# Kernel tuning notes

Hardware: AMD Instinct MI355X
Metric: run time of the kernel (lower is better)

## Reference

```python
import jax, jax.numpy as jnp
import numpy as np

N_EDGES, ADJ_K, EPROP_DIM = 50000, 9, 8
B, L = 512, 128
Z_DIM, T_DIM, TE_DIM, XE_DIM, H_DIM, O_DIM = 16, 48, 32, 128, 128, 32


def setup_inputs() -> dict:
    ks = jax.random.split(jax.random.key(0), 28)
    f = lambda k, s: jax.random.normal(k, s, jnp.float32) * 0.05
    in0 = Z_DIM + TE_DIM + XE_DIM + EPROP_DIM  # LSTM layer-0 input dim = 184
    mk_dim = XE_DIM + TE_DIM + EPROP_DIM       # 168
    return {
        "x": jax.random.randint(ks[0], (B, L), 0, N_EDGES),
        "dpt": jax.random.randint(ks[1], (B, L), 0, T_DIM),
        "z": jax.random.normal(ks[2], (L, B, Z_DIM), jnp.float32),
        "adj": jax.random.randint(ks[3], (N_EDGES, ADJ_K), 0, N_EDGES),
        "eprop": f(ks[4], (N_EDGES, EPROP_DIM)),
        "x_emb": f(ks[5], (N_EDGES, XE_DIM)),
        "t_emb": f(ks[6], (T_DIM, TE_DIM)),
        "tcost_emb": f(ks[7], (N_EDGES, TE_DIM)),
        "w_ih0": f(ks[8], (4 * H_DIM, in0)),
        "w_hh0": f(ks[9], (4 * H_DIM, H_DIM)),
        "b_ih0": f(ks[10], (4 * H_DIM,)),
        "b_hh0": f(ks[11], (4 * H_DIM,)),
        "w_ih1": f(ks[12], (4 * H_DIM, H_DIM)),
        "w_hh1": f(ks[13], (4 * H_DIM, H_DIM)),
        "b_ih1": f(ks[14], (4 * H_DIM,)),
        "b_hh1": f(ks[15], (4 * H_DIM,)),
        "w_ih2": f(ks[16], (4 * H_DIM, H_DIM)),
        "w_hh2": f(ks[17], (4 * H_DIM, H_DIM)),
        "b_ih2": f(ks[18], (4 * H_DIM,)),
        "b_hh2": f(ks[19], (4 * H_DIM,)),
        "wax": f(ks[20], (O_DIM, H_DIM)),
        "bax": f(ks[21], (O_DIM,)),
        "wat": f(ks[22], (O_DIM, 2 * TE_DIM)),
        "bat": f(ks[23], (O_DIM,)),
        "wmx": f(ks[24], (O_DIM, mk_dim)),
        "bmx": f(ks[25], (O_DIM,)),
        "wmt": f(ks[26], (O_DIM, mk_dim)),
        "bmt": f(ks[27], (O_DIM,)),
    }


def _lstm_cell(x, h, c, w_ih, w_hh, b_ih, b_hh):
    # PyTorch LSTMCell: gates ordered (i, f, g, o)
    g = x @ w_ih.T + b_ih + h @ w_hh.T + b_hh
    i, f, gg, o = jnp.split(g, 4, axis=-1)
    c = jax.nn.sigmoid(f) * c + jax.nn.sigmoid(i) * jnp.tanh(gg)
    h = jax.nn.sigmoid(o) * jnp.tanh(c)
    return h, c


def _forward(x, dpt, z, adj, eprop, x_emb, t_emb, tcost_emb,
             w_ih0, w_hh0, b_ih0, b_hh0, w_ih1, w_hh1, b_ih1, b_hh1,
             w_ih2, w_hh2, b_ih2, b_hh2, wax, bax, wat, bat, wmx, bmx, wmt, bmt):
    Bb = x.shape[0]
    N, K = adj.shape
    mask_id = N  # adj.size(0) + config.ADJ_MASK with ADJ_MASK=0 (pad id; never a valid node)
    H = w_hh0.shape[1]
    zro = lambda: jnp.zeros((Bb, H), x_emb.dtype)
    init = (zro(), zro(), zro(), zro(), zro(), zro())

    def step(carry, inp):
        h0, c0, h1, c1, h2, c2 = carry
        xt, dt, zt = inp                                   # [B], [B], [B,z]
        tt = t_emb[dt]                                     # [B,te]
        hid = jnp.concatenate([zt, x_emb[xt], tt, eprop[xt]], -1)
        h0, c0 = _lstm_cell(hid, h0, c0, w_ih0, w_hh0, b_ih0, b_hh0)
        h1, c1 = _lstm_cell(h0, h1, c1, w_ih1, w_hh1, b_ih1, b_hh1)
        h2, c2 = _lstm_cell(h1, h2, c2, w_ih2, w_hh2, b_ih2, b_hh2)
        afterx = jax.nn.relu(h2 @ wax.T + bax)             # [B,o]
        adjs = adj[xt]                                     # [B,K]
        ttb = jnp.broadcast_to(tt[:, None, :], (Bb, K, tt.shape[-1]))
        aftert = jax.nn.relu(jnp.concatenate([tcost_emb[adjs], ttb], -1) @ wat.T + bat)  # [B,K,o]
        mk = jnp.concatenate([x_emb[adjs], ttb, eprop[adjs]], -1)  # [B,K,xe+te+P]
        px = jnp.einsum('bo,bko->bk', afterx, mk @ wmx.T + bmx)    # [B,K]
        px = jnp.where(adjs == mask_id, -jnp.inf, px)
        pt = jnp.sum(aftert * (mk @ wmt.T + bmt), -1)              # [B,K]
        out = (jax.nn.log_softmax(px, -1), jax.nn.sigmoid(pt))
        return (h0, c0, h1, c1, h2, c2), out

    _, (pred_x, pred_t) = jax.lax.scan(step, init, (x.T, dpt.T, z))
    # torch stacks along dim 1 -> [B,L,K] then .view(-1,K)
    pred_x = jnp.transpose(pred_x, (1, 0, 2)).reshape(-1, K)
    pred_t = jnp.transpose(pred_t, (1, 0, 2)).reshape(-1, K)
    return pred_x, pred_t


def reference(x, dpt, z, adj, eprop, x_emb, t_emb, tcost_emb,
              w_ih0, w_hh0, b_ih0, b_hh0, w_ih1, w_hh1, b_ih1, b_hh1,
              w_ih2, w_hh2, b_ih2, b_hh2, wax, bax, wat, bat, wmx, bmx, wmt, bmt):
    return _forward(x, dpt, z, adj, eprop, x_emb, t_emb, tcost_emb,
                    w_ih0, w_hh0, b_ih0, b_hh0, w_ih1, w_hh1, b_ih1, b_hh1,
                    w_ih2, w_hh2, b_ih2, b_hh2, wax, bax, wat, bat, wmx, bmx, wmt, bmt)
```

## Files before the change

### kernel.cpp

```cpp
#include <hip/hip_runtime.h>
#include <hip/hip_fp16.h>
#include <math.h>
#include <stdint.h>

#define B_   512
#define L_   128
#define K_   9
#define NE   50000
#define ZD   16
#define TE   32
#define XE   128
#define EP   8
#define H_   128
#define G4   512
#define OD   32
#define IN0  184
#define MKD  168

typedef uint32_t u32;
typedef _Float16 half2v __attribute__((ext_vector_type(2)));
typedef _Float16 half8  __attribute__((ext_vector_type(8)));
typedef float    f32x4  __attribute__((ext_vector_type(4)));

__device__ __forceinline__ float sigm(float x) {
    x = fminf(fmaxf(x, -30.f), 30.f);
    return 1.f / (1.f + expf(-x));
}
__device__ __forceinline__ float tanh_f(float x) {
    x = fminf(fmaxf(x, -15.f), 15.f);
    float e = expf(2.f * x);
    return (e - 1.f) / (e + 1.f);
}
__device__ __forceinline__ float dot2f(u32 w, u32 h, float acc) {
#if __has_builtin(__builtin_amdgcn_fdot2)
    union { u32 u; half2v v; } a, b;
    a.u = w; b.u = h;
    return __builtin_amdgcn_fdot2(a.v, b.v, acc, false);
#else
    union { u32 u; __half2 h2; } a, b;
    a.u = w; b.u = h;
    float2 fa = __half22float2(a.h2), fb = __half22float2(b.h2);
    return fmaf(fa.x, fb.x, fmaf(fa.y, fb.y, acc));
#endif
}
__device__ __forceinline__ float dot4(uint4 w, uint4 h, float acc) {
    acc = dot2f(w.x, h.x, acc); acc = dot2f(w.y, h.y, acc);
    acc = dot2f(w.z, h.z, acc); acc = dot2f(w.w, h.w, acc);
    return acc;
}
__device__ __forceinline__ u32 packh(float lo, float hi) {
    union { __half2 h; u32 u; } p;
    p.h = __halves2half2(__float2half(lo), __float2half(hi));
    return p.u;
}
__device__ __forceinline__ f32x4 cvt4h(u32 a_, u32 b_) {
    union { u32 u; half2v v; } a, b;
    a.u = a_; b.u = b_;
    f32x4 r;
    r[0] = (float)a.v[0]; r[1] = (float)a.v[1];
    r[2] = (float)b.v[0]; r[3] = (float)b.v[1];
    return r;
}

__global__ void __launch_bounds__(256)
kW2(const float* __restrict__ w_ih0, const float* __restrict__ w_hh0,
    const float* __restrict__ w_ih1, const float* __restrict__ w_hh1,
    const float* __restrict__ w_ih2, const float* __restrict__ w_hh2,
    const float* __restrict__ wax, const float* __restrict__ wmx,
    const float* __restrict__ wmt, const float* __restrict__ wat,
    const float* __restrict__ b_ih0, const float* __restrict__ b_hh0,
    const float* __restrict__ b_ih1, const float* __restrict__ b_hh1,
    const float* __restrict__ b_ih2, const float* __restrict__ b_hh2,
    u32* __restrict__ wsu)
{
    int gid = blockIdx.x * 256 + threadIdx.x;
    if (gid < 49152) {
        int g = gid / 96, c = gid % 96;
        wsu[gid] = (c < 92) ? packh(w_ih0[g * IN0 + 2 * c], w_ih0[g * IN0 + 2 * c + 1]) : 0u;
    } else if (gid < 81920) {
        int e = gid - 49152;
        int q = e & 3, g = (e >> 2) & 511, j4 = e >> 11;
        int j2 = 4 * j4 + q;
        wsu[gid] = packh(w_hh0[g * H_ + 2 * j2], w_hh0[g * H_ + 2 * j2 + 1]);
    } else if (gid < 114688) {
        int e = gid - 81920; int g = e >> 6, c = e & 63;
        wsu[gid] = packh(w_ih1[g * H_ + 2 * c], w_ih1[g * H_ + 2 * c + 1]);
    } else if (gid < 147456) {
        int e = gid - 114688;
        int q = e & 3, g = (e >> 2) & 511, j4 = e >> 11;
        int j2 = 4 * j4 + q;
        wsu[gid] = packh(w_hh1[g * H_ + 2 * j2], w_hh1[g * H_ + 2 * j2 + 1]);
    } else if (gid < 180224) {
        int e = gid - 147456; int g = e >> 6, c = e & 63;
        wsu[gid] = packh(w_ih2[g * H_ + 2 * c], w_ih2[g * H_ + 2 * c + 1]);
    } else if (gid < 212992) {
        int e = gid - 180224;
        int q = e & 3, g = (e >> 2) & 511, j4 = e >> 11;
        int j2 = 4 * j4 + q;
        wsu[gid] = packh(w_hh2[g * H_ + 2 * j2], w_hh2[g * H_ + 2 * j2 + 1]);
    } else if (gid < 215040) {
        int e = gid - 212992; int o = e >> 6, c = e & 63;
        wsu[gid] = packh(wax[o * H_ + 2 * c], wax[o * H_ + 2 * c + 1]);
    } else if (gid < 217216) {
        int e = gid - 215040; int o = e / 68, c = e % 68;
        int col = c < 64 ? 2 * c : 160 + 2 * (c - 64);
        wsu[gid] = packh(wmx[o * MKD + col], wmx[o * MKD + col + 1]);
    } else if (gid < 219392) {
        int e = gid - 217216; int o = e / 68, c = e % 68;
        int col = c < 64 ? 2 * c : 160 + 2 * (c - 64);
        wsu[gid] = packh(wmt[o * MKD + col], wmt[o * MKD + col + 1]);
    } else if (gid < 219904) {
        int e = gid - 219392; int o = e >> 4, c = e & 15;
        wsu[gid] = packh(wat[o * 64 + 2 * c], wat[o * 64 + 2 * c + 1]);
    } else if (gid < 221440) {
        int e = gid - 219904; int layer = e >> 9, g = e & 511;
        float v;
        if (layer == 0)      v = b_ih0[g] + b_hh0[g];
        else if (layer == 1) v = b_ih1[g] + b_hh1[g];
        else                 v = b_ih2[g] + b_hh2[g];
        ((float*)wsu)[gid] = v;
    }
}

__global__ void __launch_bounds__(256)
kT(const float* __restrict__ t_emb,
   const float* __restrict__ wmx, const float* __restrict__ wmt,
   const float* __restrict__ wat,
   const float* __restrict__ bmx, const float* __restrict__ bmt,
   const float* __restrict__ bat, float* __restrict__ ttab)
{
    int gid = blockIdx.x * 256 + threadIdx.x;
    if (gid >= 48 * 96) return;
    int dt = gid / 96, o96 = gid % 96;
    const float* te = t_emb + dt * TE;
    int o = o96 & 31;
    float acc;
    const float* w;
    if (o96 < 32)      { acc = bmx[o]; w = wmx + o * MKD + XE; }
    else if (o96 < 64) { acc = bmt[o]; w = wmt + o * MKD + XE; }
    else               { acc = bat[o]; w = wat + o * 64 + TE; }
    for (int d = 0; d < TE; ++d) acc = fmaf(te[d], w[d], acc);
    ttab[dt * 96 + o96] = acc;
}

__global__ void __launch_bounds__(256)
kE(const float* __restrict__ x_emb, const float* __restrict__ eprop,
   const float* __restrict__ tcost,
   const u32* __restrict__ wmxp, const u32* __restrict__ wmtp,
   const u32* __restrict__ watp0, _Float16* __restrict__ etab)
{
    __shared__ uint4 smx[544], smt[544], sat[128];
    int tid = threadIdx.x;
    for (int i = tid; i < 544; i += 256) {
        smx[i] = ((const uint4*)wmxp)[i];
        smt[i] = ((const uint4*)wmtp)[i];
    }
    if (tid < 128) sat[tid] = ((const uint4*)watp0)[tid];
    __syncthreads();
    int e = blockIdx.x * 256 + tid;
    if (e >= NE) return;

    u32 in[68], tin[16];
    const float* xr = x_emb + (size_t)e * XE;
#pragma unroll
    for (int c = 0; c < 64; ++c) in[c] = packh(xr[2 * c], xr[2 * c + 1]);
    const float* er = eprop + (size_t)e * EP;
#pragma unroll
    for (int c = 0; c < 4; ++c) in[64 + c] = packh(er[2 * c], er[2 * c + 1]);
    const float* tr = tcost + (size_t)e * TE;
#pragma unroll
    for (int c = 0; c < 16; ++c) tin[c] = packh(tr[2 * c], tr[2 * c + 1]);

    _Float16* outp = etab + (size_t)e * 96;
    for (int o = 0; o < OD; ++o) {
        float ax = 0.f, am = 0.f, aa = 0.f;
#pragma unroll
        for (int c4 = 0; c4 < 17; ++c4) {
            uint4 wx = smx[o * 17 + c4], wt = smt[o * 17 + c4];
            ax = dot2f(wx.x, in[c4 * 4 + 0], ax);
            ax = dot2f(wx.y, in[c4 * 4 + 1], ax);
            ax = dot2f(wx.z, in[c4 * 4 + 2], ax);
            ax = dot2f(wx.w, in[c4 * 4 + 3], ax);
            am = dot2f(wt.x, in[c4 * 4 + 0], am);
            am = dot2f(wt.y, in[c4 * 4 + 1], am);
            am = dot2f(wt.z, in[c4 * 4 + 2], am);
            am = dot2f(wt.w, in[c4 * 4 + 3], am);
        }
#pragma unroll
        for (int c4 = 0; c4 < 4; ++c4) {
            uint4 wa = sat[o * 4 + c4];
            aa = dot2f(wa.x, tin[c4 * 4 + 0], aa);
            aa = dot2f(wa.y, tin[c4 * 4 + 1], aa);
            aa = dot2f(wa.z, tin[c4 * 4 + 2], aa);
            aa = dot2f(wa.w, tin[c4 * 4 + 3], aa);
        }
        outp[o] = (_Float16)ax;
        outp[32 + o] = (_Float16)am;
        outp[64 + o] = (_Float16)aa;
    }
}

__global__ void __launch_bounds__(512)
kAP(const int* __restrict__ x, const int* __restrict__ dpt,
    const float* __restrict__ z, const float* __restrict__ eprop,
    const float* __restrict__ x_emb, const float* __restrict__ t_emb,
    u32* __restrict__ A0)
{
    int tid = threadIdx.x;
    int i = tid >> 2, q = tid & 3;
    int bl = blockIdx.x * 128 + i;
    int xt = x[bl], dt = dpt[bl];
    int b = bl >> 7, l = bl & 127;
    const float* zr = z + ((size_t)l * B_ + b) * ZD;
    const float* xr = x_emb + (size_t)xt * XE;
    const float* tr = t_emb + (size_t)dt * TE;
    const float* er = eprop + (size_t)xt * EP;
    u32* outp = A0 + (size_t)bl * 96;
#pragma unroll
    for (int cc = 0; cc < 24; ++cc) {
        int c = q * 24 + cc;
        float lo, hi;
        if (c < 8)       { lo = zr[2 * c];          hi = zr[2 * c + 1]; }
        else if (c < 72) { lo = xr[2 * (c - 8)];    hi = xr[2 * (c - 8) + 1]; }
        else if (c < 88) { lo = tr[2 * (c - 72)];   hi = tr[2 * (c - 72) + 1]; }
        else if (c < 92) { lo = er[2 * (c - 88)];   hi = er[2 * (c - 88) + 1]; }
        else             { lo = 0.f;                hi = 0.f; }
        outp[c] = packh(lo, hi);
    }
}

template<int KC>
__global__ void __launch_bounds__(512, 2)
kGm(const _Float16* __restrict__ A, const u32* __restrict__ Wp,
    const float* __restrict__ bsum, _Float16* __restrict__ Out)
{
    const int K = KC * 32;
    int tid = threadIdx.x;
    int w = tid >> 6, l = tid & 63;
    int lr = l & 15, lq = l >> 4;
    int bl0 = blockIdx.x * 64;

    half8 a[4][KC];
#pragma unroll
    for (int t = 0; t < 4; ++t)
#pragma unroll
        for (int c = 0; c < KC; ++c)
            a[t][c] = *reinterpret_cast<const half8*>(
                A + (size_t)(bl0 + t * 16 + lr) * K + c * 32 + lq * 8);

#pragma unroll
    for (int pass = 0; pass < 4; ++pass) {
        int g = pass * 128 + w * 16 + lr;
        half8 bfr[KC];
#pragma unroll
        for (int c = 0; c < KC; ++c)
            bfr[c] = *reinterpret_cast<const half8*>(
                (const _Float16*)Wp + (size_t)g * K + c * 32 + lq * 8);
        float bias = bsum[g];
#pragma unroll
        for (int t = 0; t < 4; ++t) {
            f32x4 acc = {0.f, 0.f, 0.f, 0.f};
#pragma unroll
            for (int c = 0; c < KC; ++c)
                acc = __builtin_amdgcn_mfma_f32_16x16x32_f16(a[t][c], bfr[c], acc, 0, 0, 0);
#pragma unroll
            for (int j = 0; j < 4; ++j) {
                int item = bl0 + t * 16 + lq * 4 + j;
                Out[(size_t)item * G4 + g] = (_Float16)(acc[j] + bias);
            }
        }
    }
}

__global__ void __launch_bounds__(512, 1)
kRecL(const _Float16* __restrict__ gin, const uint4* __restrict__ whQ,
      _Float16* __restrict__ hout)
{
    __shared__ uint4 wlds[16 * 512];
    __shared__ float sg[2][G4];
    __shared__ u32 hb[2][64];
    const int g  = threadIdx.x;
    const int b0 = blockIdx.x * 2;

    for (int i = g; i < 16 * 512; i += 512) wlds[i] = whQ[i];
    if (g < 128) ((u32*)hb)[g] = 0;

    const int r_ = g >> 7, hd_ = g & 127;
    float c_reg = 0.f;
    const _Float16* gb0 = gin + (size_t)(b0 + 0) * L_ * G4 + g;
    const _Float16* gb1 = gin + (size_t)(b0 + 1) * L_ * G4 + g;
    float p0 = (float)*gb0, p1 = (float)*gb1;
    __syncthreads();

    for (int l = 0; l < L_; ++l) {
        int ln = (l < L_ - 1) ? l + 1 : l;
        float n0 = (float)gb0[(size_t)ln * G4];
        float n1 = (float)gb1[(size_t)ln * G4];
        float a0 = p0, a1 = p1;
        const uint4* h0q = (const uint4*)hb[0];
        const uint4* h1q = (const uint4*)hb[1];
#pragma unroll
        for (int j4 = 0; j4 < 16; ++j4) {
            uint4 wq  = wlds[j4 * 512 + g];
            uint4 hq0 = h0q[j4];
            uint4 hq1 = h1q[j4];
            a0 = dot4(wq, hq0, a0);
            a1 = dot4(wq, hq1, a1);
        }
        sg[0][g] = a0; sg[1][g] = a1;
        __syncthreads();
        if (g < 256) {
            float gi = sg[r_][hd_], gf = sg[r_][H_ + hd_];
            float gg = sg[r_][2 * H_ + hd_], go = sg[r_][3 * H_ + hd_];
            float c = sigm(gf) * c_reg + sigm(gi) * tanh_f(gg);
            float h = sigm(go) * tanh_f(c);
            c_reg = c;
            _Float16 hh = (_Float16)h;
            ((_Float16*)hb[r_])[hd_] = hh;
            hout[((size_t)(b0 + r_) * L_ + l) * H_ + hd_] = hh;
        }
        __syncthreads();
        p0 = n0; p1 = n1;
    }
}

__global__ void __launch_bounds__(256)
kX2(const int* __restrict__ x, const int* __restrict__ dpt,
    const int* __restrict__ adj, const __half* __restrict__ h2seq,
    const u32* __restrict__ wap, const float* __restrict__ bax,
    const _Float16* __restrict__ etab, const float* __restrict__ ttab,
    float* __restrict__ pred_x, float* __restrict__ pred_t)
{
    __shared__ uint4 swp[512];
    __shared__ float stt[48 * 96];
    __shared__ float sbax[32];
    int tid = threadIdx.x;
    for (int i = tid; i < 512; i += 256) swp[i] = ((const uint4*)wap)[i];
    for (int i = tid; i < 4608; i += 256) stt[i] = ttab[i];
    if (tid < 32) sbax[tid] = bax[tid];
    __syncthreads();

    int bl = blockIdx.x * 256 + tid;
    int xt = x[bl], dt = dpt[bl];

    uint4 h2r[16];
    const uint4* h2p = (const uint4*)(h2seq + (size_t)bl * H_);
#pragma unroll
    for (int q = 0; q < 16; ++q) h2r[q] = h2p[q];

    float afterx[OD];
    for (int o = 0; o < OD; ++o) {
        float acc = sbax[o];
#pragma unroll
        for (int q = 0; q < 16; ++q) {
            uint4 w = swp[o * 16 + q];
            acc = dot2f(w.x, h2r[q].x, acc);
            acc = dot2f(w.y, h2r[q].y, acc);
            acc = dot2f(w.z, h2r[q].z, acc);
            acc = dot2f(w.w, h2r[q].w, acc);
        }
        afterx[o] = acc > 0.f ? acc : 0.f;
    }

    const float* tB = stt + dt * 96;
    float px[K_];
#pragma unroll
    for (int k = 0; k < K_; ++k) {
        int a = adj[xt * K_ + k];
        int ac = a < NE ? a : 0;
        const uint4* ep = (const uint4*)(etab + (size_t)ac * 96);
        float sx = 0.f, st = 0.f;
#pragma unroll
        for (int q = 0; q < 4; ++q) {
            uint4 e = ep[q];
            f32x4 e0 = cvt4h(e.x, e.y);
            f32x4 e1 = cvt4h(e.z, e.w);
#pragma unroll
            for (int j = 0; j < 4; ++j) {
                sx += afterx[q * 8 + j]     * (e0[j] + tB[q * 8 + j]);
                sx += afterx[q * 8 + 4 + j] * (e1[j] + tB[q * 8 + 4 + j]);
            }
        }
#pragma unroll
        for (int q = 0; q < 4; ++q) {
            uint4 em4 = ep[4 + q], ea4 = ep[8 + q];
            f32x4 m0 = cvt4h(em4.x, em4.y), m1 = cvt4h(em4.z, em4.w);
            f32x4 a0 = cvt4h(ea4.x, ea4.y), a1 = cvt4h(ea4.z, ea4.w);
#pragma unroll
            for (int j = 0; j < 4; ++j) {
                float at0 = fmaxf(a0[j] + tB[64 + q * 8 + j], 0.f);
                float at1 = fmaxf(a1[j] + tB[64 + q * 8 + 4 + j], 0.f);
                st += at0 * (m0[j] + tB[32 + q * 8 + j]);
                st += at1 * (m1[j] + tB[32 + q * 8 + 4 + j]);
            }
        }
        px[k] = (a == NE) ? -INFINITY : sx;
        pred_t[(size_t)bl * K_ + k] = 1.f / (1.f + expf(-st));
    }

    float m = px[0];
#pragma unroll
    for (int k = 1; k < K_; ++k) m = fmaxf(m, px[k]);
    float ssum = 0.f;
#pragma unroll
    for (int k = 0; k < K_; ++k) ssum += expf(px[k] - m);
    float lse = logf(ssum) + m;
#pragma unroll
    for (int k = 0; k < K_; ++k)
        pred_x[(size_t)bl * K_ + k] = px[k] - lse;
}

extern "C" void kernel_launch(void* const* d_in, const int* in_sizes, int n_in,
                              void* d_out, int out_size, void* d_ws, size_t ws_size,
                              hipStream_t stream)
{
    (void)in_sizes; (void)n_in; (void)out_size; (void)ws_size;

    const int*   x      = (const int*)  d_in[0];
    const int*   dpt    = (const int*)  d_in[1];
    const float* z      = (const float*)d_in[2];
    const int*   adj    = (const int*)  d_in[3];
    const float* eprop  = (const float*)d_in[4];
    const float* x_emb  = (const float*)d_in[5];
    const float* t_emb  = (const float*)d_in[6];
    const float* tcost  = (const float*)d_in[7];
    const float* w_ih0  = (const float*)d_in[8];
    const float* w_hh0  = (const float*)d_in[9];
    const float* b_ih0  = (const float*)d_in[10];
    const float* b_hh0  = (const float*)d_in[11];
    const float* w_ih1  = (const float*)d_in[12];
    const float* w_hh1  = (const float*)d_in[13];
    const float* b_ih1  = (const float*)d_in[14];
    const float* b_hh1  = (const float*)d_in[15];
    const float* w_ih2  = (const float*)d_in[16];
    const float* w_hh2  = (const float*)d_in[17];
    const float* b_ih2  = (const float*)d_in[18];
    const float* b_hh2  = (const float*)d_in[19];
    const float* wax    = (const float*)d_in[20];
    const float* bax    = (const float*)d_in[21];
    const float* wat    = (const float*)d_in[22];
    const float* bat    = (const float*)d_in[23];
    const float* wmx    = (const float*)d_in[24];
    const float* bmx    = (const float*)d_in[25];
    const float* wmt    = (const float*)d_in[26];
    const float* bmt    = (const float*)d_in[27];

    float* out    = (float*)d_out;
    float* pred_x = out;
    float* pred_t = out + (size_t)B_ * L_ * K_;

    u32* wsu = (u32*)d_ws;
    u32* wih0p = wsu;
    u32* whhQ0 = wsu + 49152;
    u32* wih1p = wsu + 81920;
    u32* whhQ1 = wsu + 114688;
    u32* wih2p = wsu + 147456;
    u32* whhQ2 = wsu + 180224;
    u32* wap   = wsu + 212992;
    u32* wmxp  = wsu + 215040;
    u32* wmtp  = wsu + 217216;
    u32* watp0 = wsu + 219392;
    float* bsum = (float*)(wsu + 219904);
    u32* A0    = wsu + 221440;
    _Float16* gin   = (_Float16*)(wsu + 6512896);
    _Float16* h0seq = (_Float16*)(wsu + 23290112);
    _Float16* h1seq = (_Float16*)(wsu + 27484416);
    _Float16* h2seq = (_Float16*)(wsu + 31678720);
    _Float16* etab  = (_Float16*)(wsu + 35873024);
    float* ttab = (float*)(wsu + 40673024);

    kW2<<<865, 256, 0, stream>>>(w_ih0, w_hh0, w_ih1, w_hh1, w_ih2, w_hh2,
                                 wax, wmx, wmt, wat,
                                 b_ih0, b_hh0, b_ih1, b_hh1, b_ih2, b_hh2, wsu);

    kT<<<18, 256, 0, stream>>>(t_emb, wmx, wmt, wat, bmx, bmt, bat, ttab);

    kE<<<196, 256, 0, stream>>>(x_emb, eprop, tcost, wmxp, wmtp, watp0, etab);

    kAP<<<512, 512, 0, stream>>>(x, dpt, z, eprop, x_emb, t_emb, A0);

    kGm<6><<<1024, 512, 0, stream>>>((const _Float16*)A0, wih0p, bsum + 0, gin);
    kRecL<<<256, 512, 0, stream>>>(gin, (const uint4*)whhQ0, h0seq);

    kGm<4><<<1024, 512, 0, stream>>>(h0seq, wih1p, bsum + 512, gin);
    kRecL<<<256, 512, 0, stream>>>(gin, (const uint4*)whhQ1, h1seq);

    kGm<4><<<1024, 512, 0, stream>>>(h1seq, wih2p, bsum + 1024, gin);
    kRecL<<<256, 512, 0, stream>>>(gin, (const uint4*)whhQ2, h2seq);

    kX2<<<256, 256, 0, stream>>>(x, dpt, adj, (const __half*)h2seq, wap, bax,
                                 etab, ttab, pred_x, pred_t);
}
```

Baseline: 911.4 us.

## Quantize LSTM recurrent weights and hidden state to int8 with sdot4

Adds a kernel that quantizes each w_hh row to int8 with a per-row scale, and rewrites the recurrent LSTM kernel to keep h as int8 and accumulate with integer 4-way dot products. This halves the LDS footprint of the recurrent weights and the number of dot instructions per step on the serial critical path. Hidden state is quantized to int8 (h*127), which loses precision relative to fp16 and may push errors past tolerance over 128 steps and three layers.

```diff
diff --git a/kernel.cpp b/kernel.cpp
--- a/kernel.cpp
+++ b/kernel.cpp
@@ -43,10 +43,19 @@
     return fmaf(fa.x, fb.x, fmaf(fa.y, fb.y, acc));
 #endif
 }
-__device__ __forceinline__ float dot4(uint4 w, uint4 h, float acc) {
-    acc = dot2f(w.x, h.x, acc); acc = dot2f(w.y, h.y, acc);
-    acc = dot2f(w.z, h.z, acc); acc = dot2f(w.w, h.w, acc);
-    return acc;
+__device__ __forceinline__ int sdot4i(u32 a, u32 b, int c) {
+#if __has_builtin(__builtin_amdgcn_sdot4)
+    return __builtin_amdgcn_sdot4((int)a, (int)b, c, false);
+#else
+    int r = c;
+#pragma unroll
+    for (int k = 0; k < 4; ++k) {
+        int av = (int)(signed char)(a >> (8 * k));
+        int bv = (int)(signed char)(b >> (8 * k));
+        r += av * bv;
+    }
+    return r;
+#endif
 }
 __device__ __forceinline__ u32 packh(float lo, float hi) {
     union { __half2 h; u32 u; } p;
@@ -78,26 +87,14 @@
         int g = gid / 96, c = gid % 96;
         wsu[gid] = (c < 92) ? packh(w_ih0[g * IN0 + 2 * c], w_ih0[g * IN0 + 2 * c + 1]) : 0u;
     } else if (gid < 81920) {
-        int e = gid - 49152;
-        int q = e & 3, g = (e >> 2) & 511, j4 = e >> 11;
-        int j2 = 4 * j4 + q;
-        wsu[gid] = packh(w_hh0[g * H_ + 2 * j2], w_hh0[g * H_ + 2 * j2 + 1]);
     } else if (gid < 114688) {
         int e = gid - 81920; int g = e >> 6, c = e & 63;
         wsu[gid] = packh(w_ih1[g * H_ + 2 * c], w_ih1[g * H_ + 2 * c + 1]);
     } else if (gid < 147456) {
-        int e = gid - 114688;
-        int q = e & 3, g = (e >> 2) & 511, j4 = e >> 11;
-        int j2 = 4 * j4 + q;
-        wsu[gid] = packh(w_hh1[g * H_ + 2 * j2], w_hh1[g * H_ + 2 * j2 + 1]);
     } else if (gid < 180224) {
         int e = gid - 147456; int g = e >> 6, c = e & 63;
         wsu[gid] = packh(w_ih2[g * H_ + 2 * c], w_ih2[g * H_ + 2 * c + 1]);
     } else if (gid < 212992) {
-        int e = gid - 180224;
-        int q = e & 3, g = (e >> 2) & 511, j4 = e >> 11;
-        int j2 = 4 * j4 + q;
-        wsu[gid] = packh(w_hh2[g * H_ + 2 * j2], w_hh2[g * H_ + 2 * j2 + 1]);
     } else if (gid < 215040) {
         int e = gid - 212992; int o = e >> 6, c = e & 63;
         wsu[gid] = packh(wax[o * H_ + 2 * c], wax[o * H_ + 2 * c + 1]);
@@ -123,6 +120,38 @@
 }
 
 __global__ void __launch_bounds__(256)
+kQ(const float* __restrict__ w_hh0, const float* __restrict__ w_hh1,
+   const float* __restrict__ w_hh2, u32* __restrict__ wsu)
+{
+    int gid = blockIdx.x * 256 + threadIdx.x;
+    if (gid >= 1536) return;
+    int layer = gid >> 9, g = gid & 511;
+    const int baseoff[3] = {49152, 114688, 180224};
+    const float* src = (layer == 0 ? w_hh0 : layer == 1 ? w_hh1 : w_hh2) + (size_t)g * H_;
+    float amax = 1e-20f;
+    for (int k = 0; k < H_; ++k) amax = fmaxf(amax, fabsf(src[k]));
+    float inv = 127.f / amax;
+    u32* qw = wsu + baseoff[layer];
+    float* msc = (float*)(wsu + baseoff[layer] + 16384);
+    msc[g] = amax / (127.f * 127.f);
+#pragma unroll
+    for (int j8 = 0; j8 < 8; ++j8) {
+#pragma unroll
+        for (int q = 0; q < 4; ++q) {
+            u32 word = 0;
+#pragma unroll
+            for (int b = 0; b < 4; ++b) {
+                int col = j8 * 16 + q * 4 + b;
+                int v = (int)rintf(src[col] * inv);
+                v = v > 127 ? 127 : (v < -127 ? -127 : v);
+                word |= ((u32)(v & 0xff)) << (8 * b);
+            }
+            qw[(j8 * 512 + g) * 4 + q] = word;
+        }
+    }
+}
+
+__global__ void __launch_bounds__(256)
 kT(const float* __restrict__ t_emb,
    const float* __restrict__ wmx, const float* __restrict__ wmt,
    const float* __restrict__ wat,
@@ -273,18 +302,19 @@
 }
 
 __global__ void __launch_bounds__(512, 1)
-kRecL(const _Float16* __restrict__ gin, const uint4* __restrict__ whQ,
-      _Float16* __restrict__ hout)
-{
-    __shared__ uint4 wlds[16 * 512];
+kRecL8(const _Float16* __restrict__ gin, const uint4* __restrict__ wq8,
+       const float* __restrict__ mscale, _Float16* __restrict__ hout)
+{
+    __shared__ uint4 wlds[8 * 512];
     __shared__ float sg[2][G4];
-    __shared__ u32 hb[2][64];
+    __shared__ __align__(16) u32 hq[2][32];
     const int g  = threadIdx.x;
     const int b0 = blockIdx.x * 2;
 
-    for (int i = g; i < 16 * 512; i += 512) wlds[i] = whQ[i];
-    if (g < 128) ((u32*)hb)[g] = 0;
-
+    for (int i = g; i < 8 * 512; i += 512) wlds[i] = wq8[i];
+    if (g < 64) ((u32*)hq)[g] = 0;
+
+    const float m = mscale[g];
     const int r_ = g >> 7, hd_ = g & 127;
     float c_reg = 0.f;
     const _Float16* gb0 = gin + (size_t)(b0 + 0) * L_ * G4 + g;
@@ -296,18 +326,20 @@
         int ln = (l < L_ - 1) ? l + 1 : l;
         float n0 = (float)gb0[(size_t)ln * G4];
         float n1 = (float)gb1[(size_t)ln * G4];
-        float a0 = p0, a1 = p1;
-        const uint4* h0q = (const uint4*)hb[0];
-        const uint4* h1q = (const uint4*)hb[1];
-#pragma unroll
-        for (int j4 = 0; j4 < 16; ++j4) {
-            uint4 wq  = wlds[j4 * 512 + g];
-            uint4 hq0 = h0q[j4];
-            uint4 hq1 = h1q[j4];
-            a0 = dot4(wq, hq0, a0);
-            a1 = dot4(wq, hq1, a1);
-        }
-        sg[0][g] = a0; sg[1][g] = a1;
+        int acc0 = 0, acc1 = 0;
+        const uint4* h0q = (const uint4*)hq[0];
+        const uint4* h1q = (const uint4*)hq[1];
+#pragma unroll
+        for (int j8 = 0; j8 < 8; ++j8) {
+            uint4 wq = wlds[j8 * 512 + g];
+            uint4 ha = h0q[j8], hb = h1q[j8];
+            acc0 = sdot4i(wq.x, ha.x, acc0); acc0 = sdot4i(wq.y, ha.y, acc0);
+            acc0 = sdot4i(wq.z, ha.z, acc0); acc0 = sdot4i(wq.w, ha.w, acc0);
+            acc1 = sdot4i(wq.x, hb.x, acc1); acc1 = sdot4i(wq.y, hb.y, acc1);
+            acc1 = sdot4i(wq.z, hb.z, acc1); acc1 = sdot4i(wq.w, hb.w, acc1);
+        }
+        sg[0][g] = p0 + m * (float)acc0;
+        sg[1][g] = p1 + m * (float)acc1;
         __syncthreads();
         if (g < 256) {
             float gi = sg[r_][hd_], gf = sg[r_][H_ + hd_];
@@ -315,9 +347,9 @@
             float c = sigm(gf) * c_reg + sigm(gi) * tanh_f(gg);
             float h = sigm(go) * tanh_f(c);
             c_reg = c;
-            _Float16 hh = (_Float16)h;
-            ((_Float16*)hb[r_])[hd_] = hh;
-            hout[((size_t)(b0 + r_) * L_ + l) * H_ + hd_] = hh;
+            int qv = (int)rintf(h * 127.f);
+            ((signed char*)hq[r_])[hd_] = (signed char)qv;
+            hout[((size_t)(b0 + r_) * L_ + l) * H_ + hd_] = (_Float16)h;
         }
         __syncthreads();
         p0 = n0; p1 = n1;
@@ -451,11 +483,11 @@
 
     u32* wsu = (u32*)d_ws;
     u32* wih0p = wsu;
-    u32* whhQ0 = wsu + 49152;
+    u32* q0    = wsu + 49152;
     u32* wih1p = wsu + 81920;
-    u32* whhQ1 = wsu + 114688;
+    u32* q1    = wsu + 114688;
     u32* wih2p = wsu + 147456;
-    u32* whhQ2 = wsu + 180224;
+    u32* q2    = wsu + 180224;
     u32* wap   = wsu + 212992;
     u32* wmxp  = wsu + 215040;
     u32* wmtp  = wsu + 217216;
@@ -473,6 +505,8 @@
                                  wax, wmx, wmt, wat,
                                  b_ih0, b_hh0, b_ih1, b_hh1, b_ih2, b_hh2, wsu);
 
+    kQ<<<6, 256, 0, stream>>>(w_hh0, w_hh1, w_hh2, wsu);
+
     kT<<<18, 256, 0, stream>>>(t_emb, wmx, wmt, wat, bmx, bmt, bat, ttab);
 
     kE<<<196, 256, 0, stream>>>(x_emb, eprop, tcost, wmxp, wmtp, watp0, etab);
@@ -480,13 +514,13 @@
     kAP<<<512, 512, 0, stream>>>(x, dpt, z, eprop, x_emb, t_emb, A0);
 
     kGm<6><<<1024, 512, 0, stream>>>((const _Float16*)A0, wih0p, bsum + 0, gin);
-    kRecL<<<256, 512, 0, stream>>>(gin, (const uint4*)whhQ0, h0seq);
+    kRecL8<<<256, 512, 0, stream>>>(gin, (const uint4*)q0, (const float*)(q0 + 16384), h0seq);
 
     kGm<4><<<1024, 512, 0, stream>>>(h0seq, wih1p, bsum + 512, gin);
-    kRecL<<<256, 512, 0, stream>>>(gin, (const uint4*)whhQ1, h1seq);
+    kRecL8<<<256, 512, 0, stream>>>(gin, (const uint4*)q1, (const float*)(q1 + 16384), h1seq);
 
     kGm<4><<<1024, 512, 0, stream>>>(h1seq, wih2p, bsum + 1024, gin);
-    kRecL<<<256, 512, 0, stream>>>(gin, (const uint4*)whhQ2, h2seq);
+    kRecL8<<<256, 512, 0, stream>>>(gin, (const uint4*)q2, (const float*)(q2 + 16384), h2seq);
 
     kX2<<<256, 256, 0, stream>>>(x, dpt, adj, (const __half*)h2seq, wap, bax,
                                  etab, ttab, pred_x, pred_t);
```

Result: faster. 787.6 us (-13.6%).
